# Performance work log

Measured on AMD Instinct MI355X. Metric: run time of the kernel, lower is better.

## Reference

```python
import jax, jax.numpy as jnp
import numpy as np

PAD = 0  # padding token id; its embedding row is zero (padding_idx)


def setup_inputs() -> dict:
    key = jax.random.key(0)
    k1, k2, k3 = jax.random.split(key, 3)
    HOPS, VOCAB, D = 3, 50257, 128
    B, M, S = 32, 512, 6        # batch, memory slots, tokens per slot
    T, L = 128, 64              # trees per example, tokens per (flattened) tree
    # hop+1 embedding tables, normal(0, 0.1) like the torch init
    C = 0.1 * jax.random.normal(k1, (HOPS + 1, VOCAB, D), dtype=jnp.float32)
    C = C.at[:, PAD].set(0.0)   # padding_idx row = 0
    story = jax.random.randint(k2, (B, M, S), 0, VOCAB, dtype=jnp.int32)
    kb_tokens = jax.random.randint(k3, (B, T, L), 0, VOCAB, dtype=jnp.int32)
    return {"C": C, "story": story, "kb_tokens": kb_tokens}


def reference(C, story, kb_tokens):
    # C: [hops+1, V, D]; story: [B, M, S]; kb_tokens: [B, T, L]
    hops = C.shape[0] - 1
    B = story.shape[0]
    D = C.shape[-1]
    u = jnp.zeros((B, D), dtype=C.dtype)
    for hop in range(hops):
        # key memory: story slots (sum over tokens) + tree memories (sum over
        # all subtree tokens == dfs recursive sum, since PAD embeds to zero)
        m_story_A = jnp.take(C[hop], story, axis=0).sum(axis=2)       # [B,M,D]
        tree_A = jnp.take(C[hop], kb_tokens, axis=0).sum(axis=2)      # [B,T,D]
        m_A = jnp.concatenate([m_story_A, tree_A], axis=1)            # [B,M+T,D]
        prob = jax.nn.softmax(jnp.einsum("bmd,bd->bm", m_A, u), axis=1)
        # value memory with next-hop table
        m_story_C = jnp.take(C[hop + 1], story, axis=0).sum(axis=2)
        tree_C = jnp.take(C[hop + 1], kb_tokens, axis=0).sum(axis=2)
        m_C = jnp.concatenate([m_story_C, tree_C], axis=1)
        o_k = jnp.einsum("bm,bmd->bd", prob, m_C)
        u = u + o_k
    return u
```

## Files before the change

kernel.cpp:

```cpp
#include <hip/hip_runtime.h>
#include <math.h>

constexpr int HOPS  = 3;
constexpr int VOCAB = 50257;
constexpr int DIM   = 128;
constexpr int NB    = 32;
constexpr int NM    = 512;
constexpr int NS    = 6;
constexpr int NT    = 128;
constexpr int NL    = 64;
constexpr int SLOTS = NM + NT;
constexpr size_t TS = (size_t)VOCAB * DIM;
constexpr size_t TABSTRIDE = (size_t)NB * SLOTS * DIM;

constexpr size_t CH_ELEMS = (size_t)VOCAB * 3 * DIM;
constexpr int NE8 = (int)(CH_ELEMS / 8);

typedef _Float16 half8 __attribute__((ext_vector_type(8)));
typedef _Float16 half4 __attribute__((ext_vector_type(4)));

constexpr int CONV_BLOCKS  = 2048;
constexpr int STORY_BLOCKS = 2048;
constexpr int K1_BLOCKS    = CONV_BLOCKS + STORY_BLOCKS;
constexpr int TREE_BLOCKS  = NB * NT / 4;

__device__ __forceinline__ void addf4(float4& a, const float4& v) {
    a.x += v.x; a.y += v.y; a.z += v.z; a.w += v.w;
}

__global__ __launch_bounds__(256) void convert_story_k(
    const float* __restrict__ C, const int* __restrict__ story,
    _Float16* __restrict__ Ch, _Float16* __restrict__ msum)
{
    if (blockIdx.x & 1) {
        const int sb   = blockIdx.x >> 1;
        const int wave = threadIdx.x >> 6, lane = threadIdx.x & 63;
        const int h = lane >> 5, l32 = lane & 31;
        const int g = sb * 8 + wave * 2 + h;
        const int b = g >> 9, slot = g & (NM - 1);

        const int* idx = story + (size_t)g * NS;
        const int tokv = (l32 < NS) ? idx[l32] : 0;

        const float* Cb = C + TS + (size_t)l32 * 4;
        float4 a0 = {0,0,0,0}, a1 = {0,0,0,0}, a2 = {0,0,0,0};
        #pragma unroll
        for (int i = 0; i < NS; ++i) {
            const int s = __shfl(tokv, h * 32 + i);
            const float* p = Cb + (size_t)s * DIM;
            addf4(a0, *(const float4*)(p));
            addf4(a1, *(const float4*)(p + TS));
            addf4(a2, *(const float4*)(p + 2 * TS));
        }
        half4 h0, h1, h2;
        h0[0]=(_Float16)a0.x; h0[1]=(_Float16)a0.y; h0[2]=(_Float16)a0.z; h0[3]=(_Float16)a0.w;
        h1[0]=(_Float16)a1.x; h1[1]=(_Float16)a1.y; h1[2]=(_Float16)a1.z; h1[3]=(_Float16)a1.w;
        h2[0]=(_Float16)a2.x; h2[1]=(_Float16)a2.y; h2[2]=(_Float16)a2.z; h2[3]=(_Float16)a2.w;
        const size_t o = ((size_t)b * SLOTS + slot) * DIM + l32 * 4;
        *(half4*)(msum + o)                 = h0;
        *(half4*)(msum + o + TABSTRIDE)     = h1;
        *(half4*)(msum + o + 2 * TABSTRIDE) = h2;
    } else {
        const int cb = blockIdx.x >> 1;
        for (int e8 = cb * 256 + threadIdx.x; e8 < NE8; e8 += CONV_BLOCKS * 256) {
            const size_t base = (size_t)e8 * 8;
            const size_t v    = base / 384;
            const int    rem  = (int)(base % 384);
            const int    tab  = rem >> 7;
            const int    d    = rem & 127;
            const float* src = C + (size_t)(1 + tab) * TS + v * DIM + d;
            float4 f0 = *(const float4*)(src);
            float4 f1 = *(const float4*)(src + 4);
            half8 h;
            h[0]=(_Float16)f0.x; h[1]=(_Float16)f0.y; h[2]=(_Float16)f0.z; h[3]=(_Float16)f0.w;
            h[4]=(_Float16)f1.x; h[5]=(_Float16)f1.y; h[6]=(_Float16)f1.z; h[7]=(_Float16)f1.w;
            *(half8*)(Ch + base) = h;
        }
    }
}

__global__ __launch_bounds__(256) void tree_gather(
    const _Float16* __restrict__ Ch, const int* __restrict__ kb,
    _Float16* __restrict__ msum)
{
    const int wave = threadIdx.x >> 6, lane = threadIdx.x & 63;
    const int q = lane >> 4, l16 = lane & 15;
    const int g = blockIdx.x * 4 + wave;
    const int b = g >> 7, tr = g & (NT - 1);

    const int tok = kb[(size_t)g * NL + lane];

    float a0[8] = {0,0,0,0,0,0,0,0};
    float a1[8] = {0,0,0,0,0,0,0,0};
    float a2[8] = {0,0,0,0,0,0,0,0};

    #pragma unroll
    for (int i = 0; i < 16; ++i) {
        const int s = __shfl(tok, (lane & 48) + i);
        const _Float16* p = Ch + (size_t)s * (3 * DIM) + l16 * 8;
        half8 v0 = *(const half8*)(p);
        half8 v1 = *(const half8*)(p + DIM);
        half8 v2 = *(const half8*)(p + 2 * DIM);
        #pragma unroll
        for (int j = 0; j < 8; ++j) {
            a0[j] += (float)v0[j];
            a1[j] += (float)v1[j];
            a2[j] += (float)v2[j];
        }
    }
    #pragma unroll
    for (int j = 0; j < 8; ++j) {
        a0[j] += __shfl_xor(a0[j], 16); a0[j] += __shfl_xor(a0[j], 32);
        a1[j] += __shfl_xor(a1[j], 16); a1[j] += __shfl_xor(a1[j], 32);
        a2[j] += __shfl_xor(a2[j], 16); a2[j] += __shfl_xor(a2[j], 32);
    }
    if (q == 0) {
        half8 h0, h1, h2;
        #pragma unroll
        for (int j = 0; j < 8; ++j) {
            h0[j] = (_Float16)a0[j]; h1[j] = (_Float16)a1[j]; h2[j] = (_Float16)a2[j];
        }
        const size_t o = ((size_t)b * SLOTS + NM + tr) * DIM + l16 * 8;
        *(half8*)(msum + o)                 = h0;
        *(half8*)(msum + o + TABSTRIDE)     = h1;
        *(half8*)(msum + o + 2 * TABSTRIDE) = h2;
    }
}

__global__ __launch_bounds__(1024) void hops_fused(
    const _Float16* __restrict__ msum, float* __restrict__ out)
{
    const int b = blockIdx.x, t = threadIdx.x;
    const int rg = t >> 4, l16 = t & 15, wv = t >> 6, ln = t & 63;
    __shared__ float u_s[DIM];
    __shared__ float probs[SLOTS];
    __shared__ float part[64][DIM + 4];
    __shared__ float red[16];

    const _Float16* base = msum + (size_t)b * SLOTS * DIM;

    {
        float acc[8] = {0,0,0,0,0,0,0,0};
        #pragma unroll
        for (int m = rg; m < SLOTS; m += 64) {
            half8 v = *(const half8*)(base + (size_t)m * DIM + l16 * 8);
            #pragma unroll
            for (int j = 0; j < 8; ++j) acc[j] += (float)v[j];
        }
        #pragma unroll
        for (int j = 0; j < 8; ++j) part[rg][l16 * 8 + j] = acc[j];
        __syncthreads();
        if (t < DIM) {
            float s = 0.f;
            #pragma unroll
            for (int r = 0; r < 64; ++r) s += part[r][t];
            u_s[t] = s * (1.f / SLOTS);
        }
        __syncthreads();
    }

    for (int hop = 1; hop < HOPS; ++hop) {
        const _Float16* mA = base + (size_t)(hop - 1) * TABSTRIDE;
        const _Float16* mC = base + (size_t)hop * TABSTRIDE;

        #pragma unroll
        for (int m = rg; m < SLOTS; m += 64) {
            half8 v = *(const half8*)(mA + (size_t)m * DIM + l16 * 8);
            float d = 0.f;
            #pragma unroll
            for (int j = 0; j < 8; ++j) d = fmaf((float)v[j], u_s[l16 * 8 + j], d);
            d += __shfl_xor(d, 1); d += __shfl_xor(d, 2);
            d += __shfl_xor(d, 4); d += __shfl_xor(d, 8);
            if (l16 == 0) probs[m] = d;
        }
        __syncthreads();

        float s0 = (t < SLOTS) ? probs[t] : -INFINITY;
        float lmax = s0;
        #pragma unroll
        for (int off = 32; off > 0; off >>= 1) lmax = fmaxf(lmax, __shfl_xor(lmax, off));
        if (ln == 0) red[wv] = lmax;
        __syncthreads();
        lmax = red[0];
        #pragma unroll
        for (int r = 1; r < 16; ++r) lmax = fmaxf(lmax, red[r]);
        __syncthreads();
        float e0 = (t < SLOTS) ? expf(s0 - lmax) : 0.f;
        if (t < SLOTS) probs[t] = e0;
        float lsum = e0;
        #pragma unroll
        for (int off = 32; off > 0; off >>= 1) lsum += __shfl_xor(lsum, off);
        if (ln == 0) red[wv] = lsum;
        __syncthreads();
        float tot = red[0];
        #pragma unroll
        for (int r = 1; r < 16; ++r) tot += red[r];
        const float inv = 1.0f / tot;

        float acc[8] = {0,0,0,0,0,0,0,0};
        #pragma unroll
        for (int m = rg; m < SLOTS; m += 64) {
            const float p = probs[m];
            half8 v = *(const half8*)(mC + (size_t)m * DIM + l16 * 8);
            #pragma unroll
            for (int j = 0; j < 8; ++j) acc[j] = fmaf(p, (float)v[j], acc[j]);
        }
        __syncthreads();
        #pragma unroll
        for (int j = 0; j < 8; ++j) part[rg][l16 * 8 + j] = acc[j];
        __syncthreads();
        if (t < DIM) {
            float s = 0.f;
            #pragma unroll
            for (int r = 0; r < 64; ++r) s += part[r][t];
            u_s[t] += s * inv;
        }
        __syncthreads();
    }

    if (t < DIM) out[b * DIM + t] = u_s[t];
}

extern "C" void kernel_launch(void* const* d_in, const int* in_sizes, int n_in,
                              void* d_out, int out_size, void* d_ws, size_t ws_size,
                              hipStream_t stream) {
    const float* C     = (const float*)d_in[0];
    const int*   story = (const int*)d_in[1];
    const int*   kb    = (const int*)d_in[2];
    float*       out   = (float*)d_out;

    _Float16* Ch   = (_Float16*)d_ws;
    _Float16* msum = Ch + CH_ELEMS;

    convert_story_k<<<K1_BLOCKS, 256, 0, stream>>>(C, story, Ch, msum);
    tree_gather<<<TREE_BLOCKS, 256, 0, stream>>>(Ch, kb, msum);
    hops_fused<<<NB, 1024, 0, stream>>>(msum, out);
}
```

Before: 212.5 us.

## Gather story slots from fp16 interleaved table in tree gather kernel

The story-slot sums are no longer gathered from the fp32 tables inside the conversion kernel. They are now computed in the second kernel from the converted fp16 interleaved table, sharing the launch with the tree gather. This halves the bytes read per story gather and makes the conversion kernel a pure streaming pass. The cost is that story gathers must now wait for the conversion to finish rather than overlapping with it, and the story sums are built from fp16-rounded inputs.

```diff
diff --git a/kernel.cpp b/kernel.cpp
--- a/kernel.cpp
+++ b/kernel.cpp
@@ -17,110 +17,103 @@
 constexpr int NE8 = (int)(CH_ELEMS / 8);
 
 typedef _Float16 half8 __attribute__((ext_vector_type(8)));
-typedef _Float16 half4 __attribute__((ext_vector_type(4)));
-
-constexpr int CONV_BLOCKS  = 2048;
-constexpr int STORY_BLOCKS = 2048;
-constexpr int K1_BLOCKS    = CONV_BLOCKS + STORY_BLOCKS;
-constexpr int TREE_BLOCKS  = NB * NT / 4;
-
-__device__ __forceinline__ void addf4(float4& a, const float4& v) {
-    a.x += v.x; a.y += v.y; a.z += v.z; a.w += v.w;
-}
-
-__global__ __launch_bounds__(256) void convert_story_k(
-    const float* __restrict__ C, const int* __restrict__ story,
-    _Float16* __restrict__ Ch, _Float16* __restrict__ msum)
+
+constexpr int CONV_BLOCKS = 4096;
+constexpr int TREE_BLK    = NB * NT / 4;
+constexpr int STORY_BLK   = NB * NM / 16;
+constexpr int GATHER_BLOCKS = TREE_BLK + STORY_BLK;
+
+__global__ __launch_bounds__(256) void convert_k(
+    const float* __restrict__ C, _Float16* __restrict__ Ch)
 {
-    if (blockIdx.x & 1) {
-        const int sb   = blockIdx.x >> 1;
-        const int wave = threadIdx.x >> 6, lane = threadIdx.x & 63;
-        const int h = lane >> 5, l32 = lane & 31;
-        const int g = sb * 8 + wave * 2 + h;
-        const int b = g >> 9, slot = g & (NM - 1);
-
-        const int* idx = story + (size_t)g * NS;
-        const int tokv = (l32 < NS) ? idx[l32] : 0;
-
-        const float* Cb = C + TS + (size_t)l32 * 4;
-        float4 a0 = {0,0,0,0}, a1 = {0,0,0,0}, a2 = {0,0,0,0};
-        #pragma unroll
-        for (int i = 0; i < NS; ++i) {
-            const int s = __shfl(tokv, h * 32 + i);
-            const float* p = Cb + (size_t)s * DIM;
-            addf4(a0, *(const float4*)(p));
-            addf4(a1, *(const float4*)(p + TS));
-            addf4(a2, *(const float4*)(p + 2 * TS));
-        }
-        half4 h0, h1, h2;
-        h0[0]=(_Float16)a0.x; h0[1]=(_Float16)a0.y; h0[2]=(_Float16)a0.z; h0[3]=(_Float16)a0.w;
-        h1[0]=(_Float16)a1.x; h1[1]=(_Float16)a1.y; h1[2]=(_Float16)a1.z; h1[3]=(_Float16)a1.w;
-        h2[0]=(_Float16)a2.x; h2[1]=(_Float16)a2.y; h2[2]=(_Float16)a2.z; h2[3]=(_Float16)a2.w;
-        const size_t o = ((size_t)b * SLOTS + slot) * DIM + l32 * 4;
-        *(half4*)(msum + o)                 = h0;
-        *(half4*)(msum + o + TABSTRIDE)     = h1;
-        *(half4*)(msum + o + 2 * TABSTRIDE) = h2;
-    } else {
-        const int cb = blockIdx.x >> 1;
-        for (int e8 = cb * 256 + threadIdx.x; e8 < NE8; e8 += CONV_BLOCKS * 256) {
-            const size_t base = (size_t)e8 * 8;
-            const size_t v    = base / 384;
-            const int    rem  = (int)(base % 384);
-            const int    tab  = rem >> 7;
-            const int    d    = rem & 127;
-            const float* src = C + (size_t)(1 + tab) * TS + v * DIM + d;
-            float4 f0 = *(const float4*)(src);
-            float4 f1 = *(const float4*)(src + 4);
-            half8 h;
-            h[0]=(_Float16)f0.x; h[1]=(_Float16)f0.y; h[2]=(_Float16)f0.z; h[3]=(_Float16)f0.w;
-            h[4]=(_Float16)f1.x; h[5]=(_Float16)f1.y; h[6]=(_Float16)f1.z; h[7]=(_Float16)f1.w;
-            *(half8*)(Ch + base) = h;
-        }
-    }
-}
-
-__global__ __launch_bounds__(256) void tree_gather(
-    const _Float16* __restrict__ Ch, const int* __restrict__ kb,
-    _Float16* __restrict__ msum)
+    for (int e8 = blockIdx.x * 256 + threadIdx.x; e8 < NE8; e8 += CONV_BLOCKS * 256) {
+        const size_t base = (size_t)e8 * 8;
+        const size_t v    = base / 384;
+        const int    rem  = (int)(base % 384);
+        const int    tab  = rem >> 7;
+        const int    d    = rem & 127;
+        const float* src = C + (size_t)(1 + tab) * TS + v * DIM + d;
+        float4 f0 = *(const float4*)(src);
+        float4 f1 = *(const float4*)(src + 4);
+        half8 h;
+        h[0]=(_Float16)f0.x; h[1]=(_Float16)f0.y; h[2]=(_Float16)f0.z; h[3]=(_Float16)f0.w;
+        h[4]=(_Float16)f1.x; h[5]=(_Float16)f1.y; h[6]=(_Float16)f1.z; h[7]=(_Float16)f1.w;
+        *(half8*)(Ch + base) = h;
+    }
+}
+
+__global__ __launch_bounds__(256) void gather_fused(
+    const _Float16* __restrict__ Ch, const int* __restrict__ story,
+    const int* __restrict__ kb, _Float16* __restrict__ msum)
 {
     const int wave = threadIdx.x >> 6, lane = threadIdx.x & 63;
     const int q = lane >> 4, l16 = lane & 15;
-    const int g = blockIdx.x * 4 + wave;
-    const int b = g >> 7, tr = g & (NT - 1);
-
-    const int tok = kb[(size_t)g * NL + lane];
-
     float a0[8] = {0,0,0,0,0,0,0,0};
     float a1[8] = {0,0,0,0,0,0,0,0};
     float a2[8] = {0,0,0,0,0,0,0,0};
 
-    #pragma unroll
-    for (int i = 0; i < 16; ++i) {
-        const int s = __shfl(tok, (lane & 48) + i);
-        const _Float16* p = Ch + (size_t)s * (3 * DIM) + l16 * 8;
-        half8 v0 = *(const half8*)(p);
-        half8 v1 = *(const half8*)(p + DIM);
-        half8 v2 = *(const half8*)(p + 2 * DIM);
+    if ((blockIdx.x & 1) == 0) {
+        const int g = (blockIdx.x >> 1) * 4 + wave;
+        const int b = g >> 7, tr = g & (NT - 1);
+        const int tok = kb[(size_t)g * NL + lane];
+
+        #pragma unroll
+        for (int i = 0; i < 16; ++i) {
+            const int s = __shfl(tok, (lane & 48) + i);
+            const _Float16* p = Ch + (size_t)s * (3 * DIM) + l16 * 8;
+            half8 v0 = *(const half8*)(p);
+            half8 v1 = *(const half8*)(p + DIM);
+            half8 v2 = *(const half8*)(p + 2 * DIM);
+            #pragma unroll
+            for (int j = 0; j < 8; ++j) {
+                a0[j] += (float)v0[j];
+                a1[j] += (float)v1[j];
+                a2[j] += (float)v2[j];
+            }
+        }
         #pragma unroll
         for (int j = 0; j < 8; ++j) {
-            a0[j] += (float)v0[j];
-            a1[j] += (float)v1[j];
-            a2[j] += (float)v2[j];
-        }
-    }
-    #pragma unroll
-    for (int j = 0; j < 8; ++j) {
-        a0[j] += __shfl_xor(a0[j], 16); a0[j] += __shfl_xor(a0[j], 32);
-        a1[j] += __shfl_xor(a1[j], 16); a1[j] += __shfl_xor(a1[j], 32);
-        a2[j] += __shfl_xor(a2[j], 16); a2[j] += __shfl_xor(a2[j], 32);
-    }
-    if (q == 0) {
+            a0[j] += __shfl_xor(a0[j], 16); a0[j] += __shfl_xor(a0[j], 32);
+            a1[j] += __shfl_xor(a1[j], 16); a1[j] += __shfl_xor(a1[j], 32);
+            a2[j] += __shfl_xor(a2[j], 16); a2[j] += __shfl_xor(a2[j], 32);
+        }
+        if (q == 0) {
+            half8 h0, h1, h2;
+            #pragma unroll
+            for (int j = 0; j < 8; ++j) {
+                h0[j]=(_Float16)a0[j]; h1[j]=(_Float16)a1[j]; h2[j]=(_Float16)a2[j];
+            }
+            const size_t o = ((size_t)b * SLOTS + NM + tr) * DIM + l16 * 8;
+            *(half8*)(msum + o)                 = h0;
+            *(half8*)(msum + o + TABSTRIDE)     = h1;
+            *(half8*)(msum + o + 2 * TABSTRIDE) = h2;
+        }
+    } else {
+        const int g = (blockIdx.x >> 1) * 16 + wave * 4 + q;
+        const int b = g >> 9, slot = g & (NM - 1);
+        const int* idx = story + (size_t)g * NS;
+        const int tok = (l16 < NS) ? idx[l16] : 0;
+
+        #pragma unroll
+        for (int i = 0; i < NS; ++i) {
+            const int s = __shfl(tok, (lane & 48) + i);
+            const _Float16* p = Ch + (size_t)s * (3 * DIM) + l16 * 8;
+            half8 v0 = *(const half8*)(p);
+            half8 v1 = *(const half8*)(p + DIM);
+            half8 v2 = *(const half8*)(p + 2 * DIM);
+            #pragma unroll
+            for (int j = 0; j < 8; ++j) {
+                a0[j] += (float)v0[j];
+                a1[j] += (float)v1[j];
+                a2[j] += (float)v2[j];
+            }
+        }
         half8 h0, h1, h2;
         #pragma unroll
         for (int j = 0; j < 8; ++j) {
-            h0[j] = (_Float16)a0[j]; h1[j] = (_Float16)a1[j]; h2[j] = (_Float16)a2[j];
-        }
-        const size_t o = ((size_t)b * SLOTS + NM + tr) * DIM + l16 * 8;
+            h0[j]=(_Float16)a0[j]; h1[j]=(_Float16)a1[j]; h2[j]=(_Float16)a2[j];
+        }
+        const size_t o = ((size_t)b * SLOTS + slot) * DIM + l16 * 8;
         *(half8*)(msum + o)                 = h0;
         *(half8*)(msum + o + TABSTRIDE)     = h1;
         *(half8*)(msum + o + 2 * TABSTRIDE) = h2;
@@ -232,7 +225,7 @@
     _Float16* Ch   = (_Float16*)d_ws;
     _Float16* msum = Ch + CH_ELEMS;
 
-    convert_story_k<<<K1_BLOCKS, 256, 0, stream>>>(C, story, Ch, msum);
-    tree_gather<<<TREE_BLOCKS, 256, 0, stream>>>(Ch, kb, msum);
+    convert_k<<<CONV_BLOCKS, 256, 0, stream>>>(C, Ch);
+    gather_fused<<<GATHER_BLOCKS, 256, 0, stream>>>(Ch, story, kb, msum);
     hops_fused<<<NB, 1024, 0, stream>>>(msum, out);
 }
```

Result: no change. 213.7 us (+0.6%).
